# Optimization experiments

Hardware: AMD Instinct MI355X
Metric: run time of the kernel (lower is better)

## Reference

```python
import jax, jax.numpy as jnp
import numpy as np

MB, C, D, QS, OUT, H = 64, 24, 8, 128, 28, 256
IN = 2 * (C + 2) + QS  # 180


def _lin(k, out_d, in_d):
    kw, kb = jax.random.split(k)
    W = jax.random.normal(kw, (out_d, in_d), jnp.float32) * 0.02
    b = jax.random.normal(kb, (out_d,), jnp.float32) * 0.02
    return W, b


def setup_inputs() -> dict:
    key = jax.random.key(0)
    ks = jax.random.split(key, 10)
    x = jax.random.normal(ks[0], (MB, C, D, D), jnp.float32)
    qst = jax.random.normal(ks[1], (MB, QS), jnp.float32)
    Wg1, bg1 = _lin(ks[2], H, IN)
    Wg2, bg2 = _lin(ks[3], H, H)
    Wg3, bg3 = _lin(ks[4], H, H)
    Wg4, bg4 = _lin(ks[5], H, H)
    Wf1, bf1 = _lin(ks[6], H, H)
    Wf2, bf2 = _lin(ks[7], H, H)
    Wf3, bf3 = _lin(ks[8], OUT, H)
    return dict(x=x, qst=qst, Wg1=Wg1, bg1=bg1, Wg2=Wg2, bg2=bg2,
                Wg3=Wg3, bg3=bg3, Wg4=Wg4, bg4=bg4,
                Wf1=Wf1, bf1=bf1, Wf2=Wf2, bf2=bf2, Wf3=Wf3, bf3=bf3)


def reference(x, qst, Wg1, bg1, Wg2, bg2, Wg3, bg3, Wg4, bg4,
              Wf1, bf1, Wf2, bf2, Wf3, bf3):
    mb, c, d, _ = x.shape
    s2 = d * d
    # coord tensor (faithful to torch LongTensor integer-division semantics)
    a = jnp.arange(s2)
    cx = ((a // d - d // 2) / (d / 2.0)).astype(x.dtype)
    cy = ((a % d - d // 2) / (d / 2.0)).astype(x.dtype)
    coord = jnp.stack([cx, cy], axis=1)  # [s2, 2]
    # [mb, s2, c+2]
    x_flat = jnp.concatenate([x.reshape(mb, c, s2).transpose(0, 2, 1),
                              jnp.broadcast_to(coord, (mb, s2, 2))], axis=2)
    # x_j carries the question embedding: [mb, s2, c+2+QS]
    x_j = jnp.concatenate([x_flat,
                           jnp.broadcast_to(qst[:, None, :], (mb, s2, qst.shape[1]))], axis=2)
    # pairwise features: pair[b, p, q] = concat(x_flat[b, q], x_j[b, p])  -> [mb, s2, s2, IN]
    xi = jnp.broadcast_to(x_flat[:, None, :, :], (mb, s2, s2, x_flat.shape[-1]))
    xjb = jnp.broadcast_to(x_j[:, :, None, :], (mb, s2, s2, x_j.shape[-1]))
    pair = jnp.concatenate([xi, xjb], axis=-1)
    h = jax.nn.relu(pair @ Wg1.T + bg1)
    h = jax.nn.relu(h @ Wg2.T + bg2)
    h = jax.nn.relu(h @ Wg3.T + bg3)
    h = jax.nn.relu(h @ Wg4.T + bg4)
    # sum over all d^4 pairs -> [mb, 256]
    x_g = h.sum(axis=(1, 2))
    # f MLP (dropout is identity in eval / reference mode)
    f = jax.nn.relu(x_g @ Wf1.T + bf1)
    f = jax.nn.relu(f @ Wf2.T + bf2)
    logits = f @ Wf3.T + bf3
    return jax.nn.log_softmax(logits, axis=-1)
```

## Files before the change

kernel.cpp:

```cpp
#include <hip/hip_runtime.h>

typedef short bf16x8 __attribute__((ext_vector_type(8)));
typedef float f32x4 __attribute__((ext_vector_type(4)));

__device__ __forceinline__ unsigned short f2bf(float f) {
  union { float f; unsigned u; } v; v.f = f;
  unsigned r = v.u + 0x7fffu + ((v.u >> 16) & 1u);
  return (unsigned short)(r >> 16);
}

__device__ __forceinline__ int xidx(int m, int h) {
  return (m << 8) + (h ^ ((m & 7) << 3));
}
__device__ __forceinline__ int widx(int n, int kk) {
  return (n << 5) + (kk ^ (((n >> 1) & 3) << 3));
}

__device__ __forceinline__ void gload_lds16(void* lds, const void* g) {
  __builtin_amdgcn_global_load_lds(
      (const __attribute__((address_space(1))) unsigned int*)g,
      (__attribute__((address_space(3))) unsigned int*)lds, 16, 0, 0);
}

__global__ __launch_bounds__(256) void prep_kernel(
    const float* __restrict__ x, const float* __restrict__ qst,
    const float* __restrict__ Wg1, const float* __restrict__ bg1,
    float* __restrict__ u, float* __restrict__ v, float* __restrict__ xg)
{
  const int b = blockIdx.x;
  const int qc = blockIdx.y;
  const int h = threadIdx.x;
  if (qc == 0) xg[(b << 8) + h] = 0.f;

  __shared__ float qs_s[128];
  __shared__ float xf_s[26];
  if (h < 128) qs_s[h] = qst[(b << 7) + h];
  __syncthreads();

  const float2* wrow2 = (const float2*)(Wg1 + h * 180);
  float qv = bg1[h];
  #pragma unroll 8
  for (int j = 0; j < 64; ++j) {
    float2 w = wrow2[26 + j];
    qv += w.x * qs_s[2 * j] + w.y * qs_s[2 * j + 1];
  }

  for (int qi = 0; qi < 8; ++qi) {
    const int q = (qc << 3) + qi;
    __syncthreads();
    if (h < 24)       xf_s[h]  = x[((b * 24 + h) << 6) + q];
    else if (h == 24) xf_s[24] = (float)((q >> 3) - 4) * 0.25f;
    else if (h == 25) xf_s[25] = (float)((q & 7) - 4) * 0.25f;
    __syncthreads();
    float uv = 0.f, vv = qv;
    #pragma unroll
    for (int j = 0; j < 13; ++j) {
      float2 wa = wrow2[j];
      float2 wb = wrow2[13 + j];
      uv += wa.x * xf_s[2 * j] + wa.y * xf_s[2 * j + 1];
      vv += wb.x * xf_s[2 * j] + wb.y * xf_s[2 * j + 1];
    }
    u[(((b << 6) + q) << 8) + h] = uv;
    v[(((b << 6) + q) << 8) + h] = vv;
  }
}

__global__ __launch_bounds__(256) void wconv_kernel(
    const float* __restrict__ Wg2, const float* __restrict__ Wg3,
    const float* __restrict__ Wg4, unsigned short* __restrict__ out)
{
  int i = blockIdx.x * 256 + threadIdx.x;
  int layer = i >> 16, r = i & 65535;
  int n = r >> 8, k = r & 255;
  const float* W = (layer == 0) ? Wg2 : (layer == 1) ? Wg3 : Wg4;
  int kc = k >> 5, kk = k & 31;
  out[(layer << 16) + (kc << 13) + widx(n, kk)] = f2bf(W[r]);
}

__global__ __launch_bounds__(512) void g_mlp_kernel(
    const float* __restrict__ u, const float* __restrict__ v,
    const unsigned short* __restrict__ Wc,
    const float* __restrict__ bg2, const float* __restrict__ bg3,
    const float* __restrict__ bg4,
    float* __restrict__ xg)
{
  __shared__ unsigned short Xs[32768];
  __shared__ unsigned short Wb[2][8192];

  const int t = threadIdx.x;
  const int wg = blockIdx.x;
  const int b = wg >> 5;
  const int p0 = (wg & 31) << 1;
  const int lane = t & 63;
  const int wid = t >> 6;
  const int wr = wid >> 2, wc = wid & 3;
  const int l15 = lane & 15, l16 = lane >> 4;

  {
    const char* src = (const char*)Wc;
    gload_lds16(&Wb[0][t * 8],        src + t * 16);
    gload_lds16(&Wb[0][4096 + t * 8], src + 8192 + t * 16);
  }

  {
    const int h0 = (t & 31) << 3;
    const int mb_ = t >> 5;
    #pragma unroll
    for (int it = 0; it < 8; ++it) {
      const int m = (it << 4) + mb_;
      const int q = m & 63, p = p0 + (m >> 6);
      const float4* up = (const float4*)(u + ((((b << 6) + q) << 8) + h0));
      const float4* vp = (const float4*)(v + ((((b << 6) + p) << 8) + h0));
      float4 u0 = up[0], u1 = up[1];
      float4 v0 = vp[0], v1 = vp[1];
      union { unsigned short o[8]; uint4 vec; } pk;
      pk.o[0] = f2bf(fmaxf(u0.x + v0.x, 0.f));
      pk.o[1] = f2bf(fmaxf(u0.y + v0.y, 0.f));
      pk.o[2] = f2bf(fmaxf(u0.z + v0.z, 0.f));
      pk.o[3] = f2bf(fmaxf(u0.w + v0.w, 0.f));
      pk.o[4] = f2bf(fmaxf(u1.x + v1.x, 0.f));
      pk.o[5] = f2bf(fmaxf(u1.y + v1.y, 0.f));
      pk.o[6] = f2bf(fmaxf(u1.z + v1.z, 0.f));
      pk.o[7] = f2bf(fmaxf(u1.w + v1.w, 0.f));
      *(uint4*)&Xs[xidx(m, h0)] = pk.vec;
    }
  }
  __syncthreads();

  const int arow = (wr << 6) + l15;
  const int asw  = (l15 & 7) << 3;
  const int bko  = (l16 << 3) ^ (((l15 >> 1) & 3) << 3);

  int cur = 0;
  for (int layer = 0; layer < 3; ++layer) {
    const float* bgl = (layer == 0) ? bg2 : (layer == 1) ? bg3 : bg4;

    f32x4 acc[4][4];
    #pragma unroll
    for (int mi = 0; mi < 4; ++mi)
      #pragma unroll
      for (int ni = 0; ni < 4; ++ni)
        acc[mi][ni] = (f32x4){0.f, 0.f, 0.f, 0.f};

    for (int kc = 0; kc < 8; ++kc) {
      const int tt = (layer << 3) + kc;
      if (tt < 23) {
        const char* src = (const char*)Wc + ((tt + 1) << 14);
        unsigned short* dst = Wb[cur ^ 1];
        gload_lds16(&dst[t * 8],        src + t * 16);
        gload_lds16(&dst[4096 + t * 8], src + 8192 + t * 16);
      }
      const int kpart = (kc << 5) + (l16 << 3);
      bf16x8 a[4], bb[4];
      #pragma unroll
      for (int mi = 0; mi < 4; ++mi)
        a[mi] = *(const bf16x8*)&Xs[((arow + (mi << 4)) << 8) + (kpart ^ asw)];
      #pragma unroll
      for (int ni = 0; ni < 4; ++ni) {
        const int n = (wc << 6) + (ni << 4) + l15;
        bb[ni] = *(const bf16x8*)&Wb[cur][(n << 5) + bko];
      }
      __builtin_amdgcn_s_setprio(1);
      #pragma unroll
      for (int mi = 0; mi < 4; ++mi)
        #pragma unroll
        for (int ni = 0; ni < 4; ++ni)
          acc[mi][ni] = __builtin_amdgcn_mfma_f32_16x16x32_bf16(
              a[mi], bb[ni], acc[mi][ni], 0, 0, 0);
      __builtin_amdgcn_s_setprio(0);
      __syncthreads();
      cur ^= 1;
    }

    float bias[4];
    #pragma unroll
    for (int ni = 0; ni < 4; ++ni)
      bias[ni] = bgl[(wc << 6) + (ni << 4) + l15];

    if (layer < 2) {
      #pragma unroll
      for (int mi = 0; mi < 4; ++mi) {
        const int gm0 = (wr << 6) + (mi << 4) + (l16 << 2);
        #pragma unroll
        for (int ni = 0; ni < 4; ++ni) {
          const int gn = (wc << 6) + (ni << 4) + l15;
          #pragma unroll
          for (int r = 0; r < 4; ++r)
            Xs[xidx(gm0 + r, gn)] = f2bf(fmaxf(acc[mi][ni][r] + bias[ni], 0.f));
        }
      }
      __syncthreads();
    } else {
      #pragma unroll
      for (int ni = 0; ni < 4; ++ni) {
        float s = 0.f;
        #pragma unroll
        for (int mi = 0; mi < 4; ++mi)
          #pragma unroll
          for (int r = 0; r < 4; ++r)
            s += fmaxf(acc[mi][ni][r] + bias[ni], 0.f);
        s += __shfl_xor(s, 16);
        s += __shfl_xor(s, 32);
        if (l16 == 0)
          atomicAdd(&xg[(b << 8) + (wc << 6) + (ni << 4) + l15], s);
      }
    }
  }
}

__global__ __launch_bounds__(256) void f_mlp_kernel(
    const float* __restrict__ xg,
    const float* __restrict__ Wf1, const float* __restrict__ bf1,
    const float* __restrict__ Wf2, const float* __restrict__ bf2,
    const float* __restrict__ Wf3, const float* __restrict__ bf3,
    float* __restrict__ out)
{
  const int b = blockIdx.x, t = threadIdx.x;
  __shared__ float s0[256], s1[256];
  __shared__ float lg[28];
  s0[t] = xg[(b << 8) + t];
  __syncthreads();
  {
    const float4* w4 = (const float4*)(Wf1 + (t << 8));
    float acc = bf1[t];
    #pragma unroll 8
    for (int k = 0; k < 64; ++k) {
      float4 w = w4[k];
      acc += w.x * s0[4*k] + w.y * s0[4*k+1] + w.z * s0[4*k+2] + w.w * s0[4*k+3];
    }
    s1[t] = fmaxf(acc, 0.f);
  }
  __syncthreads();
  {
    const float4* w4 = (const float4*)(Wf2 + (t << 8));
    float acc = bf2[t];
    #pragma unroll 8
    for (int k = 0; k < 64; ++k) {
      float4 w = w4[k];
      acc += w.x * s1[4*k] + w.y * s1[4*k+1] + w.z * s1[4*k+2] + w.w * s1[4*k+3];
    }
    s0[t] = fmaxf(acc, 0.f);
  }
  __syncthreads();
  if (t < 28) {
    const float4* w4 = (const float4*)(Wf3 + (t << 8));
    float acc = bf3[t];
    for (int k = 0; k < 64; ++k) {
      float4 w = w4[k];
      acc += w.x * s0[4*k] + w.y * s0[4*k+1] + w.z * s0[4*k+2] + w.w * s0[4*k+3];
    }
    lg[t] = acc;
  }
  __syncthreads();
  if (t == 0) {
    float mx = lg[0];
    for (int i = 1; i < 28; ++i) mx = fmaxf(mx, lg[i]);
    float sum = 0.f;
    for (int i = 0; i < 28; ++i) sum += expf(lg[i] - mx);
    float lse = mx + logf(sum);
    for (int i = 0; i < 28; ++i) out[b * 28 + i] = lg[i] - lse;
  }
}

extern "C" void kernel_launch(void* const* d_in, const int* in_sizes, int n_in,
                              void* d_out, int out_size, void* d_ws, size_t ws_size,
                              hipStream_t stream) {
  (void)in_sizes; (void)n_in; (void)out_size; (void)ws_size;
  const float* x   = (const float*)d_in[0];
  const float* qst = (const float*)d_in[1];
  const float* Wg1 = (const float*)d_in[2];
  const float* bg1 = (const float*)d_in[3];
  const float* Wg2 = (const float*)d_in[4];
  const float* bg2 = (const float*)d_in[5];
  const float* Wg3 = (const float*)d_in[6];
  const float* bg3 = (const float*)d_in[7];
  const float* Wg4 = (const float*)d_in[8];
  const float* bg4 = (const float*)d_in[9];
  const float* Wf1 = (const float*)d_in[10];
  const float* bf1 = (const float*)d_in[11];
  const float* Wf2 = (const float*)d_in[12];
  const float* bf2 = (const float*)d_in[13];
  const float* Wf3 = (const float*)d_in[14];
  const float* bf3 = (const float*)d_in[15];
  float* out = (float*)d_out;

  char* ws = (char*)d_ws;
  float* u           = (float*)(ws);
  float* v           = (float*)(ws + (4u << 20));
  float* xg          = (float*)(ws + (8u << 20));
  unsigned short* Wc = (unsigned short*)(ws + (8u << 20) + (64u << 10));

  prep_kernel<<<dim3(64, 8), 256, 0, stream>>>(x, qst, Wg1, bg1, u, v, xg);
  wconv_kernel<<<768, 256, 0, stream>>>(Wg2, Wg3, Wg4, Wc);
  g_mlp_kernel<<<2048, 512, 0, stream>>>(u, v, Wc, bg2, bg3, bg4, xg);
  f_mlp_kernel<<<64, 256, 0, stream>>>(xg, Wf1, bf1, Wf2, bf2, Wf3, bf3, out);
}
```

Before: 279.7 us.

## Double g-MLP row tile to 256 pairs per block and rework prep kernel

The g-MLP kernel now handles 4 p-rows (256 pair rows) per workgroup instead of 2, so each warp computes 8x4 MFMA tiles. Each weight chunk loaded into LDS is therefore reused over twice as many rows, and half as many blocks are launched. The cost is LDS use rising to 128KB for activations plus 32KB for weights, and 128 accumulator registers per thread, which lowers occupancy to about one block per CU. The prep kernel is also collapsed to one block per batch item that caches x and the Wg1 row slices in registers and LDS, removing the per-q barriers.

```diff
diff --git a/kernel.cpp b/kernel.cpp
--- a/kernel.cpp
+++ b/kernel.cpp
@@ -28,13 +28,13 @@
     float* __restrict__ u, float* __restrict__ v, float* __restrict__ xg)
 {
   const int b = blockIdx.x;
-  const int qc = blockIdx.y;
   const int h = threadIdx.x;
-  if (qc == 0) xg[(b << 8) + h] = 0.f;
+  xg[(b << 8) + h] = 0.f;
 
   __shared__ float qs_s[128];
-  __shared__ float xf_s[26];
+  __shared__ float xs_s[24 * 64];
   if (h < 128) qs_s[h] = qst[(b << 7) + h];
+  for (int i = h; i < 1536; i += 256) xs_s[i] = x[b * 1536 + i];
   __syncthreads();
 
   const float2* wrow2 = (const float2*)(Wg1 + h * 180);
@@ -45,20 +45,24 @@
     qv += w.x * qs_s[2 * j] + w.y * qs_s[2 * j + 1];
   }
 
-  for (int qi = 0; qi < 8; ++qi) {
-    const int q = (qc << 3) + qi;
-    __syncthreads();
-    if (h < 24)       xf_s[h]  = x[((b * 24 + h) << 6) + q];
-    else if (h == 24) xf_s[24] = (float)((q >> 3) - 4) * 0.25f;
-    else if (h == 25) xf_s[25] = (float)((q & 7) - 4) * 0.25f;
-    __syncthreads();
-    float uv = 0.f, vv = qv;
+  float wa[26], wb[26];
+  #pragma unroll
+  for (int j = 0; j < 13; ++j) {
+    float2 a = wrow2[j], c = wrow2[13 + j];
+    wa[2 * j] = a.x; wa[2 * j + 1] = a.y;
+    wb[2 * j] = c.x; wb[2 * j + 1] = c.y;
+  }
+
+  for (int q = 0; q < 64; ++q) {
+    const float cxv = (float)((q >> 3) - 4) * 0.25f;
+    const float cyv = (float)((q & 7) - 4) * 0.25f;
+    float uv = wa[24] * cxv + wa[25] * cyv;
+    float vv = qv + wb[24] * cxv + wb[25] * cyv;
     #pragma unroll
-    for (int j = 0; j < 13; ++j) {
-      float2 wa = wrow2[j];
-      float2 wb = wrow2[13 + j];
-      uv += wa.x * xf_s[2 * j] + wa.y * xf_s[2 * j + 1];
-      vv += wb.x * xf_s[2 * j] + wb.y * xf_s[2 * j + 1];
+    for (int c = 0; c < 24; ++c) {
+      const float xv = xs_s[(c << 6) + q];
+      uv += wa[c] * xv;
+      vv += wb[c] * xv;
     }
     u[(((b << 6) + q) << 8) + h] = uv;
     v[(((b << 6) + q) << 8) + h] = vv;
@@ -84,13 +88,13 @@
     const float* __restrict__ bg4,
     float* __restrict__ xg)
 {
-  __shared__ unsigned short Xs[32768];
+  __shared__ unsigned short Xs[65536];
   __shared__ unsigned short Wb[2][8192];
 
   const int t = threadIdx.x;
   const int wg = blockIdx.x;
-  const int b = wg >> 5;
-  const int p0 = (wg & 31) << 1;
+  const int b = wg >> 4;
+  const int p0 = (wg & 15) << 2;
   const int lane = t & 63;
   const int wid = t >> 6;
   const int wr = wid >> 2, wc = wid & 3;
@@ -106,7 +110,7 @@
     const int h0 = (t & 31) << 3;
     const int mb_ = t >> 5;
     #pragma unroll
-    for (int it = 0; it < 8; ++it) {
+    for (int it = 0; it < 16; ++it) {
       const int m = (it << 4) + mb_;
       const int q = m & 63, p = p0 + (m >> 6);
       const float4* up = (const float4*)(u + ((((b << 6) + q) << 8) + h0));
@@ -127,7 +131,7 @@
   }
   __syncthreads();
 
-  const int arow = (wr << 6) + l15;
+  const int arow = (wr << 7) + l15;
   const int asw  = (l15 & 7) << 3;
   const int bko  = (l16 << 3) ^ (((l15 >> 1) & 3) << 3);
 
@@ -135,9 +139,9 @@
   for (int layer = 0; layer < 3; ++layer) {
     const float* bgl = (layer == 0) ? bg2 : (layer == 1) ? bg3 : bg4;
 
-    f32x4 acc[4][4];
+    f32x4 acc[8][4];
     #pragma unroll
-    for (int mi = 0; mi < 4; ++mi)
+    for (int mi = 0; mi < 8; ++mi)
       #pragma unroll
       for (int ni = 0; ni < 4; ++ni)
         acc[mi][ni] = (f32x4){0.f, 0.f, 0.f, 0.f};
@@ -151,18 +155,18 @@
         gload_lds16(&dst[4096 + t * 8], src + 8192 + t * 16);
       }
       const int kpart = (kc << 5) + (l16 << 3);
-      bf16x8 a[4], bb[4];
-      #pragma unroll
-      for (int mi = 0; mi < 4; ++mi)
-        a[mi] = *(const bf16x8*)&Xs[((arow + (mi << 4)) << 8) + (kpart ^ asw)];
+      bf16x8 a[8], bb[4];
       #pragma unroll
       for (int ni = 0; ni < 4; ++ni) {
         const int n = (wc << 6) + (ni << 4) + l15;
         bb[ni] = *(const bf16x8*)&Wb[cur][(n << 5) + bko];
       }
+      #pragma unroll
+      for (int mi = 0; mi < 8; ++mi)
+        a[mi] = *(const bf16x8*)&Xs[((arow + (mi << 4)) << 8) + (kpart ^ asw)];
       __builtin_amdgcn_s_setprio(1);
       #pragma unroll
-      for (int mi = 0; mi < 4; ++mi)
+      for (int mi = 0; mi < 8; ++mi)
         #pragma unroll
         for (int ni = 0; ni < 4; ++ni)
           acc[mi][ni] = __builtin_amdgcn_mfma_f32_16x16x32_bf16(
@@ -179,8 +183,8 @@
 
     if (layer < 2) {
       #pragma unroll
-      for (int mi = 0; mi < 4; ++mi) {
-        const int gm0 = (wr << 6) + (mi << 4) + (l16 << 2);
+      for (int mi = 0; mi < 8; ++mi) {
+        const int gm0 = (wr << 7) + (mi << 4) + (l16 << 2);
         #pragma unroll
         for (int ni = 0; ni < 4; ++ni) {
           const int gn = (wc << 6) + (ni << 4) + l15;
@@ -195,7 +199,7 @@
       for (int ni = 0; ni < 4; ++ni) {
         float s = 0.f;
         #pragma unroll
-        for (int mi = 0; mi < 4; ++mi)
+        for (int mi = 0; mi < 8; ++mi)
           #pragma unroll
           for (int r = 0; r < 4; ++r)
             s += fmaxf(acc[mi][ni][r] + bias[ni], 0.f);
@@ -290,8 +294,8 @@
   float* xg          = (float*)(ws + (8u << 20));
   unsigned short* Wc = (unsigned short*)(ws + (8u << 20) + (64u << 10));
 
-  prep_kernel<<<dim3(64, 8), 256, 0, stream>>>(x, qst, Wg1, bg1, u, v, xg);
+  prep_kernel<<<64, 256, 0, stream>>>(x, qst, Wg1, bg1, u, v, xg);
   wconv_kernel<<<768, 256, 0, stream>>>(Wg2, Wg3, Wg4, Wc);
-  g_mlp_kernel<<<2048, 512, 0, stream>>>(u, v, Wc, bg2, bg3, bg4, xg);
+  g_mlp_kernel<<<1024, 512, 0, stream>>>(u, v, Wc, bg2, bg3, bg4, xg);
   f_mlp_kernel<<<64, 256, 0, stream>>>(xg, Wf1, bf1, Wf2, bf2, Wf3, bf3, out);
 }
```

Result: slower. 388.1 us (+38.8%).
